# Optimization experiments

Hardware: AMD Instinct MI355X
Metric: run time of the kernel (lower is better)

The kernel has to match this reference:

```python
import jax, jax.numpy as jnp
import numpy as np

EPS = 1e-5

def ternary_quantize(w):
    # per-output-row abs-mean scale, round/clamp to {-1,0,1}, rescale
    scale = jnp.clip(jnp.mean(jnp.abs(w), axis=1, keepdims=True), EPS, None)
    q = jnp.clip(jnp.round(w / scale), -1.0, 1.0)
    return q * scale

def setup_inputs() -> dict:
    key = jax.random.key(0)
    k1, k2 = jax.random.split(key)
    x = jax.random.normal(k1, (8192, 4096), dtype=jnp.float32)
    weight = jax.random.normal(k2, (4096, 4096), dtype=jnp.float32) * 0.02
    return {"x": x, "weight": weight}

def reference(x, weight):
    qw = ternary_quantize(weight)          # [out, in]
    return x @ qw.T                         # [tokens, out]
```

## Files before the change

### kernel.cpp

```cpp
#include <hip/hip_runtime.h>
#include <hip/hip_bf16.h>
#include <stdint.h>

#define M_DIM 8192
#define K_DIM 4096
#define N_DIM 4096

typedef __attribute__((ext_vector_type(8))) short short8;
typedef __attribute__((ext_vector_type(4))) float floatx4;

__global__ void row_scale_kernel(const float* __restrict__ w, float* __restrict__ scales) {
    int row = blockIdx.x;
    const float4* wr = (const float4*)(w + (size_t)row * K_DIM);
    double s = 0.0;
    for (int i = threadIdx.x; i < K_DIM / 4; i += 256) {
        float4 v = wr[i];
        s += (double)fabsf(v.x) + (double)fabsf(v.y) + (double)fabsf(v.z) + (double)fabsf(v.w);
    }
    #pragma unroll
    for (int off = 32; off > 0; off >>= 1) s += __shfl_down(s, off);
    __shared__ double partial[4];
    int wave = threadIdx.x >> 6;
    if ((threadIdx.x & 63) == 0) partial[wave] = s;
    __syncthreads();
    if (threadIdx.x == 0) {
        double t = partial[0] + partial[1] + partial[2] + partial[3];
        float m = (float)(t / (double)K_DIM);
        scales[row] = fmaxf(m, 1e-5f);
    }
}

__global__ void quant_kernel(const float* __restrict__ w, const float* __restrict__ scales,
                             __hip_bfloat16* __restrict__ qb) {
    int v = blockIdx.x * blockDim.x + threadIdx.x;
    float4 wv = ((const float4*)w)[v];
    float s = scales[v >> 10];
    float q0 = fminf(fmaxf(rintf(wv.x / s), -1.f), 1.f);
    float q1 = fminf(fmaxf(rintf(wv.y / s), -1.f), 1.f);
    float q2 = fminf(fmaxf(rintf(wv.z / s), -1.f), 1.f);
    float q3 = fminf(fmaxf(rintf(wv.w / s), -1.f), 1.f);
    __hip_bfloat16 o[4] = {__float2bfloat16(q0), __float2bfloat16(q1),
                           __float2bfloat16(q2), __float2bfloat16(q3)};
    *(uint2*)(qb + 4 * (size_t)v) = *(uint2*)o;
}

__global__ void xconv_kernel(const float* __restrict__ x, __hip_bfloat16* __restrict__ xb) {
    int v = blockIdx.x * blockDim.x + threadIdx.x;
    float4 xv = ((const float4*)x)[v];
    __hip_bfloat16 o[4] = {__float2bfloat16(xv.x), __float2bfloat16(xv.y),
                           __float2bfloat16(xv.z), __float2bfloat16(xv.w)};
    *(uint2*)(xb + 4 * (size_t)v) = *(uint2*)o;
}

__device__ __forceinline__ void load16(const void* g, void* l) {
    __builtin_amdgcn_global_load_lds((const __attribute__((address_space(1))) uint32_t*)g,
                                     (__attribute__((address_space(3))) uint32_t*)l, 16, 0, 0);
}

__global__ __launch_bounds__(256) void gemm_kernel(const __hip_bfloat16* __restrict__ xb,
                                                   const __hip_bfloat16* __restrict__ qb,
                                                   const float* __restrict__ scales,
                                                   float* __restrict__ out) {
    __shared__ __align__(16) __hip_bfloat16 lsA[128 * 32];
    __shared__ __align__(16) __hip_bfloat16 lsB[128 * 32];
    int tid = threadIdx.x;
    int lane = tid & 63;
    int wave = tid >> 6;

    int bid = blockIdx.x;
    int xcd = bid & 7;
    int loc = bid >> 3;
    int gm = loc >> 7;
    int rem = loc & 127;
    int n_idx = rem >> 2;
    int m_idx = (rem & 3) + gm * 4;
    int m0 = (xcd * 8 + m_idx) * 128;
    int n0 = n_idx * 128;

    int wm = (wave >> 1) * 64;
    int wn = (wave & 1) * 64;

    floatx4 acc[4][4] = {};

    int lr = lane & 15;
    int q = lane >> 4;

    int c0 = tid;
    int c1 = tid + 256;
    int r0 = c0 >> 2, o0 = (((c0 & 3) ^ ((r0 >> 1) & 3))) * 8;
    int r1 = c1 >> 2, o1 = (((c1 & 3) ^ ((r1 >> 1) & 3))) * 8;

    const __hip_bfloat16* gA0 = xb + (size_t)(m0 + r0) * K_DIM + o0;
    const __hip_bfloat16* gA1 = xb + (size_t)(m0 + r1) * K_DIM + o1;
    const __hip_bfloat16* gB0 = qb + (size_t)(n0 + r0) * K_DIM + o0;
    const __hip_bfloat16* gB1 = qb + (size_t)(n0 + r1) * K_DIM + o1;

    for (int k0 = 0; k0 < K_DIM; k0 += 32) {
        load16(gA0 + k0, &lsA[c0 * 8]);
        load16(gA1 + k0, &lsA[c1 * 8]);
        load16(gB0 + k0, &lsB[c0 * 8]);
        load16(gB1 + k0, &lsB[c1 * 8]);
        __syncthreads();

        short8 a[4], b[4];
        #pragma unroll
        for (int i = 0; i < 4; i++) {
            int ra = wm + i * 16 + lr;
            int rb = wn + i * 16 + lr;
            a[i] = *(const short8*)&lsA[(ra * 4 + (q ^ ((ra >> 1) & 3))) * 8];
            b[i] = *(const short8*)&lsB[(rb * 4 + (q ^ ((rb >> 1) & 3))) * 8];
        }
        #pragma unroll
        for (int mi = 0; mi < 4; mi++)
            #pragma unroll
            for (int ni = 0; ni < 4; ni++)
                acc[mi][ni] = __builtin_amdgcn_mfma_f32_16x16x32_bf16(a[mi], b[ni], acc[mi][ni], 0, 0, 0);
        __syncthreads();
    }

    int cn = lane & 15;
    int rq = (lane >> 4) * 4;
    #pragma unroll
    for (int ni = 0; ni < 4; ni++) {
        int col = n0 + wn + ni * 16 + cn;
        float s = scales[col];
        #pragma unroll
        for (int mi = 0; mi < 4; mi++) {
            int rowb = m0 + wm + mi * 16 + rq;
            #pragma unroll
            for (int r = 0; r < 4; r++) {
                out[(size_t)(rowb + r) * N_DIM + col] = acc[mi][ni][r] * s;
            }
        }
    }
}

extern "C" void kernel_launch(void* const* d_in, const int* in_sizes, int n_in,
                              void* d_out, int out_size, void* d_ws, size_t ws_size,
                              hipStream_t stream) {
    const float* x = (const float*)d_in[0];
    const float* w = (const float*)d_in[1];
    float* out = (float*)d_out;

    char* ws = (char*)d_ws;
    __hip_bfloat16* xb = (__hip_bfloat16*)ws;
    __hip_bfloat16* qb = (__hip_bfloat16*)(ws + (size_t)M_DIM * K_DIM * 2);
    float* scales = (float*)(ws + (size_t)M_DIM * K_DIM * 2 + (size_t)N_DIM * K_DIM * 2);

    row_scale_kernel<<<N_DIM, 256, 0, stream>>>(w, scales);
    quant_kernel<<<(N_DIM * K_DIM / 4) / 256, 256, 0, stream>>>(w, scales, qb);
    xconv_kernel<<<(M_DIM * K_DIM / 4) / 256, 256, 0, stream>>>(x, xb);
    gemm_kernel<<<M_DIM / 128 * N_DIM / 128, 256, 0, stream>>>(xb, qb, scales, out);
}
```

Before: 582.7 us.

## Fuse weight scale+quant, widen x conversion, coalesce GEMM epilogue via LDS

Merges the row abs-mean and ternary quantization kernels into one that keeps the weight row in registers, avoiding a second read of the weights. The fp32-to-bf16 conversion of x now handles 8 elements per thread with 16-byte stores. The GEMM epilogue stages the scaled accumulators through per-wave LDS buffers so each row is written with float4 coalesced stores instead of scattered scalar stores. This adds LDS traffic and reuses the tile buffers after the main loop.

```diff
diff --git a/kernel.cpp b/kernel.cpp
--- a/kernel.cpp
+++ b/kernel.cpp
@@ -9,47 +9,56 @@
 typedef __attribute__((ext_vector_type(8))) short short8;
 typedef __attribute__((ext_vector_type(4))) float floatx4;
 
-__global__ void row_scale_kernel(const float* __restrict__ w, float* __restrict__ scales) {
+__global__ void fused_scale_quant(const float* __restrict__ w, float* __restrict__ scales,
+                                  __hip_bfloat16* __restrict__ qb) {
     int row = blockIdx.x;
     const float4* wr = (const float4*)(w + (size_t)row * K_DIM);
+    float4 v[4];
     double s = 0.0;
-    for (int i = threadIdx.x; i < K_DIM / 4; i += 256) {
-        float4 v = wr[i];
-        s += (double)fabsf(v.x) + (double)fabsf(v.y) + (double)fabsf(v.z) + (double)fabsf(v.w);
+    #pragma unroll
+    for (int i = 0; i < 4; i++) {
+        v[i] = wr[threadIdx.x + 256 * i];
+        s += (double)fabsf(v[i].x) + (double)fabsf(v[i].y) +
+             (double)fabsf(v[i].z) + (double)fabsf(v[i].w);
     }
     #pragma unroll
     for (int off = 32; off > 0; off >>= 1) s += __shfl_down(s, off);
     __shared__ double partial[4];
+    __shared__ float s_scale;
     int wave = threadIdx.x >> 6;
     if ((threadIdx.x & 63) == 0) partial[wave] = s;
     __syncthreads();
     if (threadIdx.x == 0) {
         double t = partial[0] + partial[1] + partial[2] + partial[3];
         float m = (float)(t / (double)K_DIM);
-        scales[row] = fmaxf(m, 1e-5f);
+        m = fmaxf(m, 1e-5f);
+        scales[row] = m;
+        s_scale = m;
+    }
+    __syncthreads();
+    float sc = s_scale;
+    __hip_bfloat16* qr = qb + (size_t)row * K_DIM;
+    #pragma unroll
+    for (int i = 0; i < 4; i++) {
+        float q0 = fminf(fmaxf(rintf(v[i].x / sc), -1.f), 1.f);
+        float q1 = fminf(fmaxf(rintf(v[i].y / sc), -1.f), 1.f);
+        float q2 = fminf(fmaxf(rintf(v[i].z / sc), -1.f), 1.f);
+        float q3 = fminf(fmaxf(rintf(v[i].w / sc), -1.f), 1.f);
+        __hip_bfloat16 o[4] = {__float2bfloat16(q0), __float2bfloat16(q1),
+                               __float2bfloat16(q2), __float2bfloat16(q3)};
+        *(uint2*)(qr + 4 * (threadIdx.x + 256 * i)) = *(uint2*)o;
     }
 }
 
-__global__ void quant_kernel(const float* __restrict__ w, const float* __restrict__ scales,
-                             __hip_bfloat16* __restrict__ qb) {
-    int v = blockIdx.x * blockDim.x + threadIdx.x;
-    float4 wv = ((const float4*)w)[v];
-    float s = scales[v >> 10];
-    float q0 = fminf(fmaxf(rintf(wv.x / s), -1.f), 1.f);
-    float q1 = fminf(fmaxf(rintf(wv.y / s), -1.f), 1.f);
-    float q2 = fminf(fmaxf(rintf(wv.z / s), -1.f), 1.f);
-    float q3 = fminf(fmaxf(rintf(wv.w / s), -1.f), 1.f);
-    __hip_bfloat16 o[4] = {__float2bfloat16(q0), __float2bfloat16(q1),
-                           __float2bfloat16(q2), __float2bfloat16(q3)};
-    *(uint2*)(qb + 4 * (size_t)v) = *(uint2*)o;
-}
-
 __global__ void xconv_kernel(const float* __restrict__ x, __hip_bfloat16* __restrict__ xb) {
-    int v = blockIdx.x * blockDim.x + threadIdx.x;
-    float4 xv = ((const float4*)x)[v];
-    __hip_bfloat16 o[4] = {__float2bfloat16(xv.x), __float2bfloat16(xv.y),
-                           __float2bfloat16(xv.z), __float2bfloat16(xv.w)};
-    *(uint2*)(xb + 4 * (size_t)v) = *(uint2*)o;
+    size_t v = (size_t)blockIdx.x * blockDim.x + threadIdx.x;
+    float4 a = ((const float4*)x)[2 * v];
+    float4 b = ((const float4*)x)[2 * v + 1];
+    __hip_bfloat16 o[8] = {__float2bfloat16(a.x), __float2bfloat16(a.y),
+                           __float2bfloat16(a.z), __float2bfloat16(a.w),
+                           __float2bfloat16(b.x), __float2bfloat16(b.y),
+                           __float2bfloat16(b.z), __float2bfloat16(b.w)};
+    *(uint4*)(xb + 8 * v) = *(uint4*)o;
 }
 
 __device__ __forceinline__ void load16(const void* g, void* l) {
@@ -61,8 +70,9 @@
                                                    const __hip_bfloat16* __restrict__ qb,
                                                    const float* __restrict__ scales,
                                                    float* __restrict__ out) {
-    __shared__ __align__(16) __hip_bfloat16 lsA[128 * 32];
-    __shared__ __align__(16) __hip_bfloat16 lsB[128 * 32];
+    __shared__ __align__(16) char smem[17408];
+    __hip_bfloat16* lsA = (__hip_bfloat16*)smem;
+    __hip_bfloat16* lsB = (__hip_bfloat16*)(smem + 8192);
     int tid = threadIdx.x;
     int lane = tid & 63;
     int wave = tid >> 6;
@@ -118,19 +128,25 @@
         __syncthreads();
     }
 
+    float* epi = (float*)smem + wave * (16 * 68);
     int cn = lane & 15;
-    int rq = (lane >> 4) * 4;
+    int qd = lane >> 4;
+    float sc[4];
     #pragma unroll
-    for (int ni = 0; ni < 4; ni++) {
-        int col = n0 + wn + ni * 16 + cn;
-        float s = scales[col];
+    for (int ni = 0; ni < 4; ni++) sc[ni] = scales[n0 + wn + ni * 16 + cn];
+
+    #pragma unroll
+    for (int mi = 0; mi < 4; mi++) {
         #pragma unroll
-        for (int mi = 0; mi < 4; mi++) {
-            int rowb = m0 + wm + mi * 16 + rq;
+        for (int ni = 0; ni < 4; ni++)
             #pragma unroll
-            for (int r = 0; r < 4; r++) {
-                out[(size_t)(rowb + r) * N_DIM + col] = acc[mi][ni][r] * s;
-            }
+            for (int r = 0; r < 4; r++)
+                epi[(qd * 4 + r) * 68 + ni * 16 + cn] = acc[mi][ni][r] * sc[ni];
+        int rowbase = m0 + wm + mi * 16;
+        #pragma unroll
+        for (int p = 0; p < 4; p++) {
+            float4 vv = *(const float4*)&epi[(p * 4 + qd) * 68 + cn * 4];
+            *(float4*)&out[(size_t)(rowbase + p * 4 + qd) * N_DIM + n0 + wn + cn * 4] = vv;
         }
     }
 }
@@ -147,8 +163,7 @@
     __hip_bfloat16* qb = (__hip_bfloat16*)(ws + (size_t)M_DIM * K_DIM * 2);
     float* scales = (float*)(ws + (size_t)M_DIM * K_DIM * 2 + (size_t)N_DIM * K_DIM * 2);
 
-    row_scale_kernel<<<N_DIM, 256, 0, stream>>>(w, scales);
-    quant_kernel<<<(N_DIM * K_DIM / 4) / 256, 256, 0, stream>>>(w, scales, qb);
-    xconv_kernel<<<(M_DIM * K_DIM / 4) / 256, 256, 0, stream>>>(x, xb);
+    fused_scale_quant<<<N_DIM, 256, 0, stream>>>(w, scales, qb);
+    xconv_kernel<<<(M_DIM * K_DIM / 8) / 256, 256, 0, stream>>>(x, xb);
     gemm_kernel<<<M_DIM / 128 * N_DIM / 128, 256, 0, stream>>>(xb, qb, scales, out);
 }
```

New measurement: 545.5 us. 6.4% less time.
